# Optimization experiments

Hardware: AMD Instinct MI355X
Metric: run time of the kernel (lower is better)

## Reference

```python
import jax, jax.numpy as jnp
import numpy as np

S = 100000   # unique_source_num
T = 20000    # unique_target_num
N = S + T    # total nodes (sources first, then targets)
E = 1000000  # edges
SRC_DIM, EMB_DIM, TGT_DIM = 256, 128, 128


def setup_inputs() -> dict:
    key = jax.random.key(0)
    ks = jax.random.split(key, 6)
    source_feat = jax.random.normal(ks[0], (N, SRC_DIM), dtype=jnp.float32)
    src_idx = jax.random.randint(ks[1], (E,), 0, S)            # edge sources in [0, S)
    dst_idx = jax.random.randint(ks[2], (E,), 0, T)            # edge targets, target-local in [0, T)
    range_list = jax.random.randint(ks[3], (T, 2), 0, S)       # unused by the math (passed through in torch)
    # x_norm divides features; keep it bounded away from 0 like real row norms
    x_norm = jax.random.uniform(ks[4], (N,), dtype=jnp.float32, minval=0.5, maxval=1.5)
    k_e, k_w = jax.random.split(ks[5])
    embed = jax.random.normal(k_e, (SRC_DIM, EMB_DIM), dtype=jnp.float32)          # Param, std=1 init
    weight = jax.random.normal(k_w, (EMB_DIM, TGT_DIM), dtype=jnp.float32) / np.sqrt(EMB_DIM)  # is_after_relu std=1/sqrt(in)
    return {"source_feat": source_feat, "src_idx": src_idx, "dst_idx": dst_idx,
            "range_list": range_list, "x_norm": x_norm, "embed": embed, "weight": weight}


def reference(source_feat, src_idx, dst_idx, range_list, x_norm, embed, weight):
    # x = (source_feat @ embed) / x_norm[:, None]   -> [N, EMB_DIM]
    x = jnp.matmul(source_feat, embed) / x_norm[:, None]
    # message + scatter-mean aggregation onto targets (sources receive no edges,
    # so aggregating directly over the T targets == aggr_out[S:] in the torch code)
    msgs = x[src_idx]                                           # [E, EMB_DIM] gather
    summed = jax.ops.segment_sum(msgs, dst_idx, num_segments=T) # [T, EMB_DIM]
    cnt = jax.ops.segment_sum(jnp.ones((E,), dtype=x.dtype), dst_idx, num_segments=T)
    aggr = summed / jnp.maximum(cnt, 1.0)[:, None]              # mean; zero-degree -> 0
    out = jnp.matmul(aggr, weight)                              # [T, TGT_DIM]
    return out
```

## Files before the change

kernel.cpp:

```cpp
#include <hip/hip_runtime.h>
#include <cstdint>
#include <cstddef>

#define S_NUM 100000
#define T_NUM 20000
#define E_NUM 1000000

#define NB   625
#define GT   32
#define CAP  2560
#define CH   2048

typedef __bf16 bf16x8 __attribute__((ext_vector_type(8)));
typedef float f32x4 __attribute__((ext_vector_type(4)));

__device__ __forceinline__ unsigned short f2bf(float f) {
  unsigned int u = __float_as_uint(f);
  u += 0x7fffu + ((u >> 16) & 1u);
  return (unsigned short)(u >> 16);
}
__device__ __forceinline__ unsigned int f2bf2(float lo, float hi) {
  return (unsigned int)f2bf(lo) | ((unsigned int)f2bf(hi) << 16);
}
__device__ __forceinline__ float bflo(unsigned int v) { return __uint_as_float(v << 16); }
__device__ __forceinline__ float bfhi(unsigned int v) { return __uint_as_float(v & 0xffff0000u); }

__global__ void k0_prep(const float* __restrict__ embed, const float* __restrict__ weight,
                        unsigned short* __restrict__ embT, unsigned short* __restrict__ wT) {
  int idx = blockIdx.x * blockDim.x + threadIdx.x;
  if (idx < 32768) {
    int n = idx & 127, k = idx >> 7;
    embT[n * 256 + k] = f2bf(embed[k * 128 + n]);
  } else {
    int j = idx - 32768;
    int n = j & 127, k = j >> 7;
    wT[n * 128 + k] = f2bf(weight[k * 128 + n]);
  }
}

__launch_bounds__(256)
__global__ void k1_gemm(const float* __restrict__ sf, const float* __restrict__ xn,
                        const unsigned short* __restrict__ embT,
                        unsigned short* __restrict__ xb) {
  __shared__ __align__(16) unsigned char smem[128 * 264 * 2];
  unsigned short (*lA)[264] = (unsigned short (*)[264])smem;
  unsigned short (*lC)[136] = (unsigned short (*)[136])smem;

  const int tid = threadIdx.x;
  const int wave = tid >> 6;
  const int lane = tid & 63;
  const int quad = lane >> 4;
  const int l15 = lane & 15;
  const int row0 = blockIdx.x * 128;

  bf16x8 fb[8][2];
#pragma unroll
  for (int kc = 0; kc < 8; ++kc)
#pragma unroll
    for (int ct = 0; ct < 2; ++ct) {
      const int n = wave * 32 + ct * 16 + l15;
      fb[kc][ct] = *(const bf16x8*)(embT + (size_t)n * 256 + kc * 32 + quad * 8);
    }

#pragma unroll
  for (int i = 0; i < 16; ++i) {
    const int idx = i * 256 + tid;
    const int row = idx >> 5;
    const int seg = idx & 31;
    const float4* g = (const float4*)(sf + (size_t)(row0 + row) * 256 + seg * 8);
    const float4 v0 = g[0];
    const float4 v1 = g[1];
    uint4 pk;
    pk.x = f2bf2(v0.x, v0.y);
    pk.y = f2bf2(v0.z, v0.w);
    pk.z = f2bf2(v1.x, v1.y);
    pk.w = f2bf2(v1.z, v1.w);
    *(uint4*)&lA[row][seg * 8] = pk;
  }
  __syncthreads();

  f32x4 acc[8][2];
#pragma unroll
  for (int i = 0; i < 8; ++i)
#pragma unroll
    for (int j = 0; j < 2; ++j) acc[i][j] = (f32x4){0.f, 0.f, 0.f, 0.f};

#pragma unroll
  for (int kc = 0; kc < 8; ++kc)
#pragma unroll
    for (int rt = 0; rt < 8; ++rt) {
      bf16x8 fa = *(const bf16x8*)&lA[rt * 16 + l15][kc * 32 + quad * 8];
      acc[rt][0] = __builtin_amdgcn_mfma_f32_16x16x32_bf16(fa, fb[kc][0], acc[rt][0], 0, 0, 0);
      acc[rt][1] = __builtin_amdgcn_mfma_f32_16x16x32_bf16(fa, fb[kc][1], acc[rt][1], 0, 0, 0);
    }
  __syncthreads();

  const int col0 = wave * 32;
#pragma unroll
  for (int rt = 0; rt < 8; ++rt) {
#pragma unroll
    for (int reg = 0; reg < 4; ++reg) {
      const int row = rt * 16 + quad * 4 + reg;
      const float inv = __builtin_amdgcn_rcpf(xn[row0 + row]);
      lC[row][col0 + l15]      = f2bf(acc[rt][0][reg] * inv);
      lC[row][col0 + 16 + l15] = f2bf(acc[rt][1][reg] * inv);
    }
  }
  __syncthreads();

#pragma unroll
  for (int p = 0; p < 8; ++p) {
    const int i = p * 256 + tid;
    const int row = i >> 4;
    const int seg = i & 15;
    const int gr = row0 + row;
    if (gr < S_NUM)
      *(uint4*)(xb + (size_t)gr * 128 + seg * 8) = *(const uint4*)&lC[row][seg * 8];
  }
}

__launch_bounds__(512)
__global__ void k2_partition(const int* __restrict__ src_idx, const int* __restrict__ dst_idx,
                             int* __restrict__ gcursor, unsigned int* __restrict__ ebuf) {
  __shared__ int bcnt[NB];
  __shared__ int gbase[NB];
  const int tid = threadIdx.x;
  for (int c = blockIdx.x; c * CH < E_NUM; c += gridDim.x) {
    const int e0 = c * CH;
    const int e1 = (e0 + CH < E_NUM) ? (e0 + CH) : E_NUM;
    for (int i = tid; i < NB; i += 512) bcnt[i] = 0;
    __syncthreads();
    for (int e = e0 + tid; e < e1; e += 512)
      atomicAdd(&bcnt[dst_idx[e] >> 5], 1);
    __syncthreads();
    for (int i = tid; i < NB; i += 512) {
      const int cnt = bcnt[i];
      gbase[i] = (cnt > 0) ? atomicAdd(&gcursor[i], cnt) : 0;
      bcnt[i] = 0;
    }
    __syncthreads();
    for (int e = e0 + tid; e < e1; e += 512) {
      const int d = dst_idx[e];
      const int s = src_idx[e];
      const int b = d >> 5;
      const int r = atomicAdd(&bcnt[b], 1);
      const int pos = gbase[b] + r;
      if (pos < CAP)
        ebuf[(size_t)b * CAP + pos] = ((unsigned int)(d & 31) << 17) | (unsigned int)s;
    }
    __syncthreads();
  }
}

__launch_bounds__(512)
__global__ void k3_fused(const int* __restrict__ gcursor, const unsigned int* __restrict__ ebuf,
                         const unsigned short* __restrict__ xb,
                         const unsigned short* __restrict__ wT,
                         float* __restrict__ out) {
  __shared__ unsigned int sls[CAP];
  __shared__ int hist[GT], scn[GT], cur[GT];
  __shared__ unsigned int Pu[GT][68];
  const int b = blockIdx.x;
  const int tid = threadIdx.x;
  const int wave = tid >> 6, lane = tid & 63;
  const int quad = lane >> 4, l15 = lane & 15;

  int n = gcursor[b];
  if (n > CAP) n = CAP;
  const unsigned int* eb = ebuf + (size_t)b * CAP;

  if (tid < GT) hist[tid] = 0;
  __syncthreads();
  for (int i = tid; i < n; i += 512) atomicAdd(&hist[eb[i] >> 17], 1);
  __syncthreads();
  if (tid == 0) {
    int run = 0;
#pragma unroll
    for (int i = 0; i < GT; ++i) { scn[i] = run; run += hist[i]; }
  }
  __syncthreads();
  if (tid < GT) cur[tid] = scn[tid];
  __syncthreads();
  for (int i = tid; i < n; i += 512) {
    const unsigned int e = eb[i];
    const int r = atomicAdd(&cur[e >> 17], 1);
    sls[r] = e & 0x1FFFFu;
  }
  __syncthreads();

#pragma unroll
  for (int rep = 0; rep < 4; ++rep) {
    const int tl = wave * 4 + rep;
    const int beg = scn[tl];
    const int c = hist[tl];
    float a0 = 0.f, a1 = 0.f, b0 = 0.f, b1 = 0.f;
    int e = 0;
    for (; e + 8 <= c; e += 8) {
      int s[8];
#pragma unroll
      for (int j = 0; j < 8; ++j) s[j] = (int)sls[beg + e + j];
      unsigned int v[8];
#pragma unroll
      for (int j = 0; j < 8; ++j)
        v[j] = *(const unsigned int*)(xb + (size_t)s[j] * 128 + 2 * lane);
#pragma unroll
      for (int j = 0; j < 8; j += 2) {
        a0 += bflo(v[j]);     a1 += bfhi(v[j]);
        b0 += bflo(v[j + 1]); b1 += bfhi(v[j + 1]);
      }
    }
    for (; e < c; ++e) {
      const int s0 = (int)sls[beg + e];
      const unsigned int v0 = *(const unsigned int*)(xb + (size_t)s0 * 128 + 2 * lane);
      a0 += bflo(v0); a1 += bfhi(v0);
    }
    a0 += b0; a1 += b1;
    const float inv = (c > 0) ? __builtin_amdgcn_rcpf((float)c) : 0.f;
    Pu[tl][lane] = f2bf2(a0 * inv, a1 * inv);
  }
  __syncthreads();

  const int ncol = wave * 16 + l15;
  bf16x8 wb[4];
#pragma unroll
  for (int kc = 0; kc < 4; ++kc)
    wb[kc] = *(const bf16x8*)(wT + (size_t)ncol * 128 + kc * 32 + quad * 8);
  f32x4 o0 = (f32x4){0.f, 0.f, 0.f, 0.f};
  f32x4 o1 = (f32x4){0.f, 0.f, 0.f, 0.f};
#pragma unroll
  for (int kc = 0; kc < 4; ++kc) {
    bf16x8 p0 = *(const bf16x8*)((const unsigned short*)&Pu[l15][0] + kc * 32 + quad * 8);
    bf16x8 p1 = *(const bf16x8*)((const unsigned short*)&Pu[16 + l15][0] + kc * 32 + quad * 8);
    o0 = __builtin_amdgcn_mfma_f32_16x16x32_bf16(p0, wb[kc], o0, 0, 0, 0);
    o1 = __builtin_amdgcn_mfma_f32_16x16x32_bf16(p1, wb[kc], o1, 0, 0, 0);
  }
#pragma unroll
  for (int reg = 0; reg < 4; ++reg) {
    out[((size_t)b * 32 + quad * 4 + reg) * 128 + ncol]      = o0[reg];
    out[((size_t)b * 32 + 16 + quad * 4 + reg) * 128 + ncol] = o1[reg];
  }
}

extern "C" void kernel_launch(void* const* d_in, const int* in_sizes, int n_in,
                              void* d_out, int out_size, void* d_ws, size_t ws_size,
                              hipStream_t stream) {
  const float* sf      = (const float*)d_in[0];
  const int*   src_idx = (const int*)d_in[1];
  const int*   dst_idx = (const int*)d_in[2];
  const float* xn      = (const float*)d_in[4];
  const float* embed   = (const float*)d_in[5];
  const float* weight  = (const float*)d_in[6];
  float* out = (float*)d_out;

  char* w = (char*)d_ws;
  unsigned short* xb   = (unsigned short*)(w);
  unsigned short* embT = (unsigned short*)(w + 25600000);
  unsigned short* wT   = (unsigned short*)(w + 25665536);
  int* gcursor         = (int*)(w + 25698304);
  unsigned int* ebuf   = (unsigned int*)(w + 25702400);

  hipMemsetAsync(gcursor, 0, 4096, stream);
  k0_prep<<<192, 256, 0, stream>>>(embed, weight, embT, wT);
  k1_gemm<<<(S_NUM + 127) / 128, 256, 0, stream>>>(sf, xn, embT, xb);
  k2_partition<<<(E_NUM + CH - 1) / CH, 512, 0, stream>>>(src_idx, dst_idx, gcursor, ebuf);
  k3_fused<<<NB, 512, 0, stream>>>(gcursor, ebuf, xb, wT, out);
}
```

Measured before the change: 266.8 us.

## Fuse GEMM and edge partition into one launch, drop prep kernel

Merges the edge-partitioning kernel and the source-feature GEMM into a single launch. The first blocks bucket edges and the rest compute the projected features, so the two independent stages can run on the GPU at the same time. The prep kernel that transposed and converted embed/weight is removed: each GEMM block and each aggregation block now reads the fp32 matrices with strided loads and converts them in-register. The GEMM block grows to 512 threads with each wave owning 16 columns, the partition chunk doubles to 4096 edges, and the gather loop is unrolled to 16 with a 4-wide tail. In exchange, every block repeats the weight conversion using uncoalesced loads, and 512-thread blocks may lower GEMM occupancy.

```diff
diff --git a/kernel.cpp b/kernel.cpp
--- a/kernel.cpp
+++ b/kernel.cpp
@@ -9,7 +9,9 @@
 #define NB   625
 #define GT   32
 #define CAP  2560
-#define CH   2048
+#define CH   4096
+#define KB2  245
+#define KB1  782
 
 typedef __bf16 bf16x8 __attribute__((ext_vector_type(8)));
 typedef float f32x4 __attribute__((ext_vector_type(4)));
@@ -25,46 +27,64 @@
 __device__ __forceinline__ float bflo(unsigned int v) { return __uint_as_float(v << 16); }
 __device__ __forceinline__ float bfhi(unsigned int v) { return __uint_as_float(v & 0xffff0000u); }
 
-__global__ void k0_prep(const float* __restrict__ embed, const float* __restrict__ weight,
-                        unsigned short* __restrict__ embT, unsigned short* __restrict__ wT) {
-  int idx = blockIdx.x * blockDim.x + threadIdx.x;
-  if (idx < 32768) {
-    int n = idx & 127, k = idx >> 7;
-    embT[n * 256 + k] = f2bf(embed[k * 128 + n]);
-  } else {
-    int j = idx - 32768;
-    int n = j & 127, k = j >> 7;
-    wT[n * 128 + k] = f2bf(weight[k * 128 + n]);
-  }
-}
-
-__launch_bounds__(256)
-__global__ void k1_gemm(const float* __restrict__ sf, const float* __restrict__ xn,
-                        const unsigned short* __restrict__ embT,
-                        unsigned short* __restrict__ xb) {
+__launch_bounds__(512)
+__global__ void k12_fused(const float* __restrict__ sf, const float* __restrict__ xn,
+                          const float* __restrict__ embed, unsigned short* __restrict__ xb,
+                          const int* __restrict__ src_idx, const int* __restrict__ dst_idx,
+                          int* __restrict__ gcursor, unsigned int* __restrict__ ebuf) {
   __shared__ __align__(16) unsigned char smem[128 * 264 * 2];
+  const int tid = threadIdx.x;
+
+  if (blockIdx.x < KB2) {
+    int* bcnt  = (int*)smem;
+    int* gbase = (int*)(smem + 2560);
+    const int e0 = blockIdx.x * CH;
+    const int e1 = (e0 + CH < E_NUM) ? (e0 + CH) : E_NUM;
+    for (int i = tid; i < NB; i += 512) bcnt[i] = 0;
+    __syncthreads();
+    for (int e = e0 + tid; e < e1; e += 512)
+      atomicAdd(&bcnt[dst_idx[e] >> 5], 1);
+    __syncthreads();
+    for (int i = tid; i < NB; i += 512) {
+      const int cnt = bcnt[i];
+      gbase[i] = (cnt > 0) ? atomicAdd(&gcursor[i], cnt) : 0;
+      bcnt[i] = 0;
+    }
+    __syncthreads();
+    for (int e = e0 + tid; e < e1; e += 512) {
+      const int d = dst_idx[e];
+      const int s = src_idx[e];
+      const int b = d >> 5;
+      const int r = atomicAdd(&bcnt[b], 1);
+      const int pos = gbase[b] + r;
+      if (pos < CAP)
+        ebuf[(size_t)b * CAP + pos] = ((unsigned int)(d & 31) << 17) | (unsigned int)s;
+    }
+    return;
+  }
+
   unsigned short (*lA)[264] = (unsigned short (*)[264])smem;
   unsigned short (*lC)[136] = (unsigned short (*)[136])smem;
-
-  const int tid = threadIdx.x;
   const int wave = tid >> 6;
   const int lane = tid & 63;
   const int quad = lane >> 4;
   const int l15 = lane & 15;
-  const int row0 = blockIdx.x * 128;
-
-  bf16x8 fb[8][2];
-#pragma unroll
-  for (int kc = 0; kc < 8; ++kc)
-#pragma unroll
-    for (int ct = 0; ct < 2; ++ct) {
-      const int n = wave * 32 + ct * 16 + l15;
-      fb[kc][ct] = *(const bf16x8*)(embT + (size_t)n * 256 + kc * 32 + quad * 8);
-    }
-
-#pragma unroll
-  for (int i = 0; i < 16; ++i) {
-    const int idx = i * 256 + tid;
+  const int row0 = (blockIdx.x - KB2) * 128;
+  const int col0 = wave * 16;
+
+  bf16x8 fb[8];
+#pragma unroll
+  for (int kc = 0; kc < 8; ++kc) {
+    union { unsigned short h[8]; bf16x8 v; } u;
+#pragma unroll
+    for (int j = 0; j < 8; ++j)
+      u.h[j] = f2bf(embed[(size_t)(kc * 32 + quad * 8 + j) * 128 + col0 + l15]);
+    fb[kc] = u.v;
+  }
+
+#pragma unroll
+  for (int i = 0; i < 8; ++i) {
+    const int idx = i * 512 + tid;
     const int row = idx >> 5;
     const int seg = idx & 31;
     const float4* g = (const float4*)(sf + (size_t)(row0 + row) * 256 + seg * 8);
@@ -79,38 +99,33 @@
   }
   __syncthreads();
 
-  f32x4 acc[8][2];
-#pragma unroll
-  for (int i = 0; i < 8; ++i)
-#pragma unroll
-    for (int j = 0; j < 2; ++j) acc[i][j] = (f32x4){0.f, 0.f, 0.f, 0.f};
+  f32x4 acc[8];
+#pragma unroll
+  for (int i = 0; i < 8; ++i) acc[i] = (f32x4){0.f, 0.f, 0.f, 0.f};
 
 #pragma unroll
   for (int kc = 0; kc < 8; ++kc)
 #pragma unroll
     for (int rt = 0; rt < 8; ++rt) {
       bf16x8 fa = *(const bf16x8*)&lA[rt * 16 + l15][kc * 32 + quad * 8];
-      acc[rt][0] = __builtin_amdgcn_mfma_f32_16x16x32_bf16(fa, fb[kc][0], acc[rt][0], 0, 0, 0);
-      acc[rt][1] = __builtin_amdgcn_mfma_f32_16x16x32_bf16(fa, fb[kc][1], acc[rt][1], 0, 0, 0);
-    }
-  __syncthreads();
-
-  const int col0 = wave * 32;
+      acc[rt] = __builtin_amdgcn_mfma_f32_16x16x32_bf16(fa, fb[kc], acc[rt], 0, 0, 0);
+    }
+  __syncthreads();
+
 #pragma unroll
   for (int rt = 0; rt < 8; ++rt) {
 #pragma unroll
     for (int reg = 0; reg < 4; ++reg) {
       const int row = rt * 16 + quad * 4 + reg;
       const float inv = __builtin_amdgcn_rcpf(xn[row0 + row]);
-      lC[row][col0 + l15]      = f2bf(acc[rt][0][reg] * inv);
-      lC[row][col0 + 16 + l15] = f2bf(acc[rt][1][reg] * inv);
-    }
-  }
-  __syncthreads();
-
-#pragma unroll
-  for (int p = 0; p < 8; ++p) {
-    const int i = p * 256 + tid;
+      lC[row][col0 + l15] = f2bf(acc[rt][reg] * inv);
+    }
+  }
+  __syncthreads();
+
+#pragma unroll
+  for (int p = 0; p < 4; ++p) {
+    const int i = p * 512 + tid;
     const int row = i >> 4;
     const int seg = i & 15;
     const int gr = row0 + row;
@@ -120,42 +135,9 @@
 }
 
 __launch_bounds__(512)
-__global__ void k2_partition(const int* __restrict__ src_idx, const int* __restrict__ dst_idx,
-                             int* __restrict__ gcursor, unsigned int* __restrict__ ebuf) {
-  __shared__ int bcnt[NB];
-  __shared__ int gbase[NB];
-  const int tid = threadIdx.x;
-  for (int c = blockIdx.x; c * CH < E_NUM; c += gridDim.x) {
-    const int e0 = c * CH;
-    const int e1 = (e0 + CH < E_NUM) ? (e0 + CH) : E_NUM;
-    for (int i = tid; i < NB; i += 512) bcnt[i] = 0;
-    __syncthreads();
-    for (int e = e0 + tid; e < e1; e += 512)
-      atomicAdd(&bcnt[dst_idx[e] >> 5], 1);
-    __syncthreads();
-    for (int i = tid; i < NB; i += 512) {
-      const int cnt = bcnt[i];
-      gbase[i] = (cnt > 0) ? atomicAdd(&gcursor[i], cnt) : 0;
-      bcnt[i] = 0;
-    }
-    __syncthreads();
-    for (int e = e0 + tid; e < e1; e += 512) {
-      const int d = dst_idx[e];
-      const int s = src_idx[e];
-      const int b = d >> 5;
-      const int r = atomicAdd(&bcnt[b], 1);
-      const int pos = gbase[b] + r;
-      if (pos < CAP)
-        ebuf[(size_t)b * CAP + pos] = ((unsigned int)(d & 31) << 17) | (unsigned int)s;
-    }
-    __syncthreads();
-  }
-}
-
-__launch_bounds__(512)
 __global__ void k3_fused(const int* __restrict__ gcursor, const unsigned int* __restrict__ ebuf,
                          const unsigned short* __restrict__ xb,
-                         const unsigned short* __restrict__ wT,
+                         const float* __restrict__ weight,
                          float* __restrict__ out) {
   __shared__ unsigned int sls[CAP];
   __shared__ int hist[GT], scn[GT], cur[GT];
@@ -195,19 +177,32 @@
     const int c = hist[tl];
     float a0 = 0.f, a1 = 0.f, b0 = 0.f, b1 = 0.f;
     int e = 0;
-    for (; e + 8 <= c; e += 8) {
-      int s[8];
-#pragma unroll
-      for (int j = 0; j < 8; ++j) s[j] = (int)sls[beg + e + j];
-      unsigned int v[8];
-#pragma unroll
-      for (int j = 0; j < 8; ++j)
+    for (; e + 16 <= c; e += 16) {
+      int s[16];
+#pragma unroll
+      for (int j = 0; j < 16; ++j) s[j] = (int)sls[beg + e + j];
+      unsigned int v[16];
+#pragma unroll
+      for (int j = 0; j < 16; ++j)
         v[j] = *(const unsigned int*)(xb + (size_t)s[j] * 128 + 2 * lane);
 #pragma unroll
-      for (int j = 0; j < 8; j += 2) {
+      for (int j = 0; j < 16; j += 2) {
         a0 += bflo(v[j]);     a1 += bfhi(v[j]);
         b0 += bflo(v[j + 1]); b1 += bfhi(v[j + 1]);
       }
+    }
+    for (; e + 4 <= c; e += 4) {
+      int s[4];
+#pragma unroll
+      for (int j = 0; j < 4; ++j) s[j] = (int)sls[beg + e + j];
+      unsigned int v[4];
+#pragma unroll
+      for (int j = 0; j < 4; ++j)
+        v[j] = *(const unsigned int*)(xb + (size_t)s[j] * 128 + 2 * lane);
+      a0 += bflo(v[0]); a1 += bfhi(v[0]);
+      b0 += bflo(v[1]); b1 += bfhi(v[1]);
+      a0 += bflo(v[2]); a1 += bfhi(v[2]);
+      b0 += bflo(v[3]); b1 += bfhi(v[3]);
     }
     for (; e < c; ++e) {
       const int s0 = (int)sls[beg + e];
@@ -223,8 +218,13 @@
   const int ncol = wave * 16 + l15;
   bf16x8 wb[4];
 #pragma unroll
-  for (int kc = 0; kc < 4; ++kc)
-    wb[kc] = *(const bf16x8*)(wT + (size_t)ncol * 128 + kc * 32 + quad * 8);
+  for (int kc = 0; kc < 4; ++kc) {
+    union { unsigned short h[8]; bf16x8 v; } u;
+#pragma unroll
+    for (int j = 0; j < 8; ++j)
+      u.h[j] = f2bf(weight[(size_t)(kc * 32 + quad * 8 + j) * 128 + ncol]);
+    wb[kc] = u.v;
+  }
   f32x4 o0 = (f32x4){0.f, 0.f, 0.f, 0.f};
   f32x4 o1 = (f32x4){0.f, 0.f, 0.f, 0.f};
 #pragma unroll
@@ -253,15 +253,11 @@
   float* out = (float*)d_out;
 
   char* w = (char*)d_ws;
-  unsigned short* xb   = (unsigned short*)(w);
-  unsigned short* embT = (unsigned short*)(w + 25600000);
-  unsigned short* wT   = (unsigned short*)(w + 25665536);
-  int* gcursor         = (int*)(w + 25698304);
-  unsigned int* ebuf   = (unsigned int*)(w + 25702400);
+  unsigned short* xb = (unsigned short*)(w);
+  int* gcursor       = (int*)(w + 25600000);
+  unsigned int* ebuf = (unsigned int*)(w + 25604096);
 
   hipMemsetAsync(gcursor, 0, 4096, stream);
-  k0_prep<<<192, 256, 0, stream>>>(embed, weight, embT, wT);
-  k1_gemm<<<(S_NUM + 127) / 128, 256, 0, stream>>>(sf, xn, embT, xb);
-  k2_partition<<<(E_NUM + CH - 1) / CH, 512, 0, stream>>>(src_idx, dst_idx, gcursor, ebuf);
-  k3_fused<<<NB, 512, 0, stream>>>(gcursor, ebuf, xb, wT, out);
-}
+  k12_fused<<<KB2 + KB1, 512, 0, stream>>>(sf, xn, embed, xb, src_idx, dst_idx, gcursor, ebuf);
+  k3_fused<<<NB, 512, 0, stream>>>(gcursor, ebuf, xb, weight, out);
+}
```

Result: faster. 255.0 us (-4.4%).
